# Performance work log

Measured on AMD Instinct MI355X. Metric: run time of the kernel, lower is better.

## Reference

```python
import jax, jax.numpy as jnp
import numpy as np

BOUND = 1.0
MIN_NEAR = 0.05
NUM_STEPS = 64
UP_STEPS = 64
DENSITY_SCALE = 1.0
N_RAYS = 16384
HIDDEN = 64


def setup_inputs() -> dict:
    key = jax.random.key(0)
    ks = jax.random.split(key, 8)
    # cameras hover near z=2 looking roughly toward -z so rays hit the [-1,1]^3 AABB
    rays_o = jax.random.normal(ks[0], (N_RAYS, 3), jnp.float32) * 0.1 + jnp.array([0.0, 0.0, 2.0])
    rays_d = jax.random.normal(ks[1], (N_RAYS, 3), jnp.float32) * 0.2 + jnp.array([0.0, 0.0, -1.0])
    rays_d = rays_d / jnp.linalg.norm(rays_d, axis=-1, keepdims=True)
    W1 = jax.random.normal(ks[2], (3, HIDDEN), jnp.float32) / jnp.sqrt(3.0)
    b1 = jnp.zeros((HIDDEN,), jnp.float32)
    w_sigma = jax.random.normal(ks[3], (HIDDEN, 1), jnp.float32) / jnp.sqrt(float(HIDDEN))
    b_sigma = jnp.zeros((1,), jnp.float32)
    W_rgb = jax.random.normal(ks[4], (HIDDEN, 3), jnp.float32) / jnp.sqrt(float(HIDDEN))
    b_rgb = jnp.zeros((3,), jnp.float32)
    return {"rays_o": rays_o, "rays_d": rays_d, "W1": W1, "b1": b1,
            "w_sigma": w_sigma, "b_sigma": b_sigma, "W_rgb": W_rgb, "b_rgb": b_rgb}


def near_far_cube(rays_o, rays_d, bound, min_near):
    tmin = (-bound - rays_o) / (rays_d + 1e-15)
    tmax = (bound - rays_o) / (rays_d + 1e-15)
    near = jnp.max(jnp.minimum(tmin, tmax), axis=-1, keepdims=True)
    far = jnp.min(jnp.maximum(tmin, tmax), axis=-1, keepdims=True)
    miss = far < near
    near = jnp.where(miss, 1e9, near)
    far = jnp.where(miss, 1e9, far)
    near = jnp.maximum(near, min_near)
    return near, far


def sample_pdf(bins, weights, n_samples):
    # bins: [N, M+1], weights: [N, M]; deterministic (det=True) inverse-CDF sampling
    weights = weights + 1e-5
    pdf = weights / jnp.sum(weights, -1, keepdims=True)
    cdf = jnp.cumsum(pdf, -1)
    cdf = jnp.concatenate([jnp.zeros_like(cdf[..., :1]), cdf], -1)  # [N, M+1]
    u = jnp.linspace(0.5 / n_samples, 1.0 - 0.5 / n_samples, n_samples, dtype=cdf.dtype)
    u = jnp.broadcast_to(u, cdf.shape[:-1] + (n_samples,))
    inds = jax.vmap(lambda c, uu: jnp.searchsorted(c, uu, side='right'))(cdf, u)
    below = jnp.maximum(inds - 1, 0)
    above = jnp.minimum(inds, cdf.shape[-1] - 1)
    cdf_b = jnp.take_along_axis(cdf, below, -1)
    cdf_a = jnp.take_along_axis(cdf, above, -1)
    bins_b = jnp.take_along_axis(bins, below, -1)
    bins_a = jnp.take_along_axis(bins, above, -1)
    denom = cdf_a - cdf_b
    denom = jnp.where(denom < 1e-5, jnp.ones_like(denom), denom)
    t = (u - cdf_b) / denom
    return bins_b + t * (bins_a - bins_b)


def mlp(pts, W1, b1, w_sigma, b_sigma, W_rgb, b_rgb):
    h = jax.nn.relu(pts @ W1 + b1)                      # [N, T, HIDDEN]
    sigma = jax.nn.softplus(h @ w_sigma + b_sigma)[..., 0]  # [N, T]
    rgb = jax.nn.sigmoid(h @ W_rgb + b_rgb)             # [N, T, 3]
    return sigma, rgb


def alpha_composite_weights(z_vals, sigma, sample_dist):
    deltas = z_vals[..., 1:] - z_vals[..., :-1]
    deltas = jnp.concatenate([deltas, jnp.broadcast_to(sample_dist, deltas[..., :1].shape)], -1)
    alphas = 1.0 - jnp.exp(-deltas * DENSITY_SCALE * sigma)
    trans = jnp.cumprod(jnp.concatenate([jnp.ones_like(alphas[..., :1]), 1.0 - alphas + 1e-15], -1)[..., :-1], -1)
    return alphas * trans


def reference(rays_o, rays_d, W1, b1, w_sigma, b_sigma, W_rgb, b_rgb):
    rays_d = rays_d / jnp.linalg.norm(rays_d, axis=-1, keepdims=True)
    near, far = near_far_cube(rays_o, rays_d, BOUND, MIN_NEAR)  # [N,1]
    sample_dist = (far - near) / NUM_STEPS                      # [N,1]

    # coarse stratified (deterministic) samples
    z = jnp.linspace(0.0, 1.0, NUM_STEPS, dtype=rays_o.dtype)
    z_vals = near + (far - near) * z                            # [N,T]
    xyzs = rays_o[:, None, :] + rays_d[:, None, :] * z_vals[..., None]
    xyzs = jnp.clip(xyzs, -BOUND, BOUND)
    sigma, _ = mlp(xyzs, W1, b1, w_sigma, b_sigma, W_rgb, b_rgb)
    weights = alpha_composite_weights(z_vals, sigma, sample_dist)

    # inverse-CDF importance resampling (no-grad in original)
    z_mid = 0.5 * (z_vals[..., :-1] + z_vals[..., 1:])          # [N,T-1]
    new_z = sample_pdf(z_mid, weights[:, 1:-1], UP_STEPS)       # [N,UP]
    new_z = jax.lax.stop_gradient(new_z)

    z_all = jnp.sort(jnp.concatenate([z_vals, new_z], -1), -1)  # [N,T+UP]
    xyzs_all = rays_o[:, None, :] + rays_d[:, None, :] * z_all[..., None]
    xyzs_all = jnp.clip(xyzs_all, -BOUND, BOUND)
    sigma_all, rgb_all = mlp(xyzs_all, W1, b1, w_sigma, b_sigma, W_rgb, b_rgb)
    weights_all = alpha_composite_weights(z_all, sigma_all, sample_dist)

    weights_sum = jnp.sum(weights_all, -1)                      # [N]
    image = jnp.sum(weights_all[..., None] * rgb_all, axis=-2)  # [N,3]
    image = image + (1.0 - weights_sum)[..., None]              # white background
    return image
```

## Files before the change

kernel.cpp:

```cpp
#include <hip/hip_runtime.h>
#include <math.h>

#define WAVES_PER_BLOCK 4

typedef float v2f __attribute__((ext_vector_type(2)));
typedef float v4f __attribute__((ext_vector_type(4)));
typedef __fp16 fp16v2 __attribute__((ext_vector_type(2)));
typedef _Float16 half8 __attribute__((ext_vector_type(8)));

__device__ __forceinline__ v2f v2_fma(v2f a, v2f b, v2f c) {
    return __builtin_elementwise_fma(a, b, c);
}
__device__ __forceinline__ v2f v2_max0(v2f a) {
    return __builtin_elementwise_max(a, (v2f){0.0f, 0.0f});
}
__device__ __forceinline__ v2f v2_splat(float x) { return (v2f){x, x}; }

__device__ __forceinline__ float fast_rcp(float x) { return __builtin_amdgcn_rcpf(x); }

#define DPP_ROW_SHR(n)  (0x110 | (n))
#define DPP_WF_SL1      0x130
#define DPP_WF_SR1      0x138
#define DPP_ROW_BCAST15 0x142
#define DPP_ROW_BCAST31 0x143

template <int CTRL, int RM = 0xf, int BM = 0xf, bool BC = false>
__device__ __forceinline__ float fdpp(float old_, float src) {
    return __int_as_float(__builtin_amdgcn_update_dpp(
        __float_as_int(old_), __float_as_int(src), CTRL, RM, BM, BC));
}
template <int CTRL, int RM = 0xf, int BM = 0xf, bool BC = false>
__device__ __forceinline__ int idpp(int old_, int src) {
    return __builtin_amdgcn_update_dpp(old_, src, CTRL, RM, BM, BC);
}

__device__ __forceinline__ float lane63_bcast(float x) {
    return __int_as_float(__builtin_amdgcn_readlane(__float_as_int(x), 63));
}

__device__ __forceinline__ float scan_add_dpp(float x) {
    x += fdpp<DPP_ROW_SHR(1)>(0.0f, x);
    x += fdpp<DPP_ROW_SHR(2)>(0.0f, x);
    x += fdpp<DPP_ROW_SHR(4)>(0.0f, x);
    x += fdpp<DPP_ROW_SHR(8)>(0.0f, x);
    x += fdpp<DPP_ROW_BCAST15, 0xa>(0.0f, x);
    x += fdpp<DPP_ROW_BCAST31, 0xc>(0.0f, x);
    return x;
}
__device__ __forceinline__ float scan_mul_dpp(float x) {
    x *= fdpp<DPP_ROW_SHR(1)>(1.0f, x);
    x *= fdpp<DPP_ROW_SHR(2)>(1.0f, x);
    x *= fdpp<DPP_ROW_SHR(4)>(1.0f, x);
    x *= fdpp<DPP_ROW_SHR(8)>(1.0f, x);
    x *= fdpp<DPP_ROW_BCAST15, 0xa>(1.0f, x);
    x *= fdpp<DPP_ROW_BCAST31, 0xc>(1.0f, x);
    return x;
}
__device__ __forceinline__ float wave_sum_dpp(float x) {
    return lane63_bcast(scan_add_dpp(x));
}
__device__ __forceinline__ int imax2(int a, int b) { return a > b ? a : b; }
__device__ __forceinline__ int imax_scan_dpp(int x) {
    const int NEG = (int)0x80000000;
    x = imax2(x, idpp<DPP_ROW_SHR(1)>(NEG, x));
    x = imax2(x, idpp<DPP_ROW_SHR(2)>(NEG, x));
    x = imax2(x, idpp<DPP_ROW_SHR(4)>(NEG, x));
    x = imax2(x, idpp<DPP_ROW_SHR(8)>(NEG, x));
    x = imax2(x, idpp<DPP_ROW_BCAST15, 0xa>(NEG, x));
    x = imax2(x, idpp<DPP_ROW_BCAST31, 0xc>(NEG, x));
    return x;
}

__device__ __forceinline__ float softplus_f(float x) {
    return fmaxf(x, 0.0f) + __logf(1.0f + __expf(-fabsf(x)));
}
__device__ __forceinline__ float sigmoid_f(float x) {
    return fast_rcp(1.0f + __expf(-x));
}
__device__ __forceinline__ float clamp1(float x) {
    return fminf(fmaxf(x, -1.0f), 1.0f);
}

__device__ __forceinline__ void bstage(float& a, float& b, int d, int lane) {
    float av = __shfl_xor(a, d, 64);
    float bv = __shfl_xor(b, d, 64);
    bool up = (lane & d) != 0;
    float alo = fminf(a, av), ahi = fmaxf(a, av);
    float blo = fminf(b, bv), bhi = fmaxf(b, bv);
    a = up ? ahi : alo;
    b = up ? bhi : blo;
}

__device__ __forceinline__ half8 build_afrag(const v2f* cr, const v2f* mr, v2f zz, int q) {
    union { half8 h; fp16v2 p[4]; } af;
#pragma unroll
    for (int g4 = 0; g4 < 4; ++g4) {
        v2f hp = v2_max0(v2_fma(mr[q * 4 + g4], zz, cr[q * 4 + g4]));
        af.p[g4] = __builtin_amdgcn_cvt_pkrtz(hp.x, hp.y);
    }
    return af.h;
}

__global__ __launch_bounds__(WAVES_PER_BLOCK * 64, 4)
void nerf_render_kernel(const float* __restrict__ rays_o,
                        const float* __restrict__ rays_d,
                        const float* __restrict__ W1,
                        const float* __restrict__ b1,
                        const float* __restrict__ w_sigma,
                        const float* __restrict__ b_sigma,
                        const float* __restrict__ W_rgb,
                        const float* __restrict__ b_rgb,
                        float* __restrict__ out)
{
    const int tid  = threadIdx.x;
    const int lane = tid & 63;
    const int wv   = tid >> 6;
    const int ray  = blockIdx.x * WAVES_PER_BLOCK + wv;
    const int r15  = lane & 15;
    const int kgrp = lane >> 4;

    __shared__ float s_cm [WAVES_PER_BLOCK][128];
    __shared__ int   s_scr[WAVES_PER_BLOCK][64];
    __shared__ float s_sig[WAVES_PER_BLOCK][64];
    __shared__ float s_out[WAVES_PER_BLOCK][4 * 132];

    half8 bfrag[2];
#pragma unroll
    for (int q = 0; q < 2; ++q) {
#pragma unroll
        for (int j = 0; j < 8; ++j) {
            int k = q * 32 + kgrp * 8 + j;
            float wval = 0.0f;
            if (r15 == 0)      wval = w_sigma[k];
            else if (r15 < 4)  wval = W_rgb[3 * k + (r15 - 1)];
            bfrag[q][j] = (_Float16)wval;
        }
    }

    float ox = rays_o[ray * 3 + 0], oy = rays_o[ray * 3 + 1], oz = rays_o[ray * 3 + 2];
    float dx = rays_d[ray * 3 + 0], dy = rays_d[ray * 3 + 1], dz = rays_d[ray * 3 + 2];
    {
        float inv = __builtin_amdgcn_rsqf(dx * dx + dy * dy + dz * dz);
        dx *= inv; dy *= inv; dz *= inv;
    }

    float rx = fast_rcp(dx + 1e-15f);
    float ry = fast_rcp(dy + 1e-15f);
    float rz = fast_rcp(dz + 1e-15f);
    float t0x = (-1.0f - ox) * rx, t1x = (1.0f - ox) * rx;
    float t0y = (-1.0f - oy) * ry, t1y = (1.0f - oy) * ry;
    float t0z = (-1.0f - oz) * rz, t1z = (1.0f - oz) * rz;
    float nearv = fmaxf(fmaxf(fminf(t0x, t1x), fminf(t0y, t1y)), fminf(t0z, t1z));
    float farv  = fminf(fminf(fmaxf(t0x, t1x), fmaxf(t0y, t1y)), fmaxf(t0z, t1z));
    const bool miss = (farv < nearv);
    if (miss) { nearv = 1e9f; farv = 1e9f; }
    nearv = fmaxf(nearv, 0.05f);
    const float sample_dist = (farv - nearv) * (1.0f / 64.0f);

    const float bs0 = b_sigma[0];
    const float br0 = b_rgb[0], br1 = b_rgb[1], br2 = b_rgb[2];

    {
        float w1x = W1[lane], w1y = W1[64 + lane], w1z = W1[128 + lane];
        float eox = ox, eoy = oy, eoz = oz, msc = 1.0f;
        if (miss) {
            eox = clamp1(fmaf(dx, 1e9f, ox));
            eoy = clamp1(fmaf(dy, 1e9f, oy));
            eoz = clamp1(fmaf(dz, 1e9f, oz));
            msc = 0.0f;
        }
        float cj = fmaf(eox, w1x, fmaf(eoy, w1y, fmaf(eoz, w1z, b1[lane])));
        float mj = msc * fmaf(dx, w1x, fmaf(dy, w1y, dz * w1z));
        int g = (lane >> 1) * 4 + (lane & 1);
        s_cm[wv][g]     = cj;
        s_cm[wv][g + 2] = mj;
    }

    v2f cr[8], mr[8];
#pragma unroll
    for (int q = 0; q < 2; ++q) {
#pragma unroll
        for (int g4 = 0; g4 < 4; ++g4) {
            v4f g = *(const v4f*)&s_cm[wv][4 * (q * 16 + kgrp * 4 + g4)];
            cr[q * 4 + g4] = (v2f){g.x, g.y};
            mr[q * 4 + g4] = (v2f){g.z, g.w};
        }
    }

    const float biasv = (r15 == 0) ? bs0 : (r15 == 1) ? br0 : (r15 == 2) ? br1
                       : (r15 == 3) ? br2 : 0.0f;
    const v4f accInit = (v4f){biasv, biasv, biasv, biasv};

    const float stepz = (farv - nearv) * (1.0f / 63.0f);
#pragma unroll
    for (int mt = 0; mt < 4; ++mt) {
        float zs = fminf(fmaf(stepz, (float)(mt * 16 + r15), nearv), 6.0e4f);
        v2f zz = v2_splat(zs);
        v4f acc = accInit;
        acc = __builtin_amdgcn_mfma_f32_16x16x32_f16(build_afrag(cr, mr, zz, 0), bfrag[0], acc, 0, 0, 0);
        acc = __builtin_amdgcn_mfma_f32_16x16x32_f16(build_afrag(cr, mr, zz, 1), bfrag[1], acc, 0, 0, 0);
        if (r15 == 0) {
            *(v4f*)&s_sig[wv][mt * 16 + kgrp * 4] = acc;
        }
    }
    float sigma = softplus_f(s_sig[wv][lane]);

    float z = nearv + (farv - nearv) * ((float)lane * (1.0f / 63.0f));

    float z_next = fdpp<DPP_WF_SL1>(0.0f, z);
    float delta  = (lane < 63) ? (z_next - z) : sample_dist;
    float alpha  = 1.0f - __expf(-delta * sigma);
    float v      = 1.0f - alpha + 1e-15f;
    float incl   = scan_mul_dpp(v);
    float trans  = fdpp<DPP_WF_SR1>(1.0f, incl);
    float w = alpha * trans;

    float wgt = (lane >= 1 && lane <= 62) ? (w + 1e-5f) : 0.0f;
    float cumw = scan_add_dpp(wgt);
    float total = lane63_bcast(cumw);
    float cdf_incl = cumw * fast_rcp(total);

    float cdfv  = (lane < 63) ? cdf_incl : 2.0f;
    float zmidv = (lane < 63) ? (0.5f * (z + z_next)) : 0.0f;

    int s = (int)ceilf(fmaf(64.0f, cdfv, -0.5f));
    s = s < 0 ? 0 : (s > 64 ? 64 : s);
    int snext = idpp<DPP_WF_SL1>(65, s);
    bool glast = (snext > s) && (s < 64);

    s_scr[wv][lane] = -1;
    if (glast) s_scr[wv][s] = lane;
    int below = imax_scan_dpp(s_scr[wv][lane]);
    int above = below + 1; if (above > 62) above = 62;

    float cb = __shfl(cdfv,  below, 64);
    float ca = __shfl(cdfv,  above, 64);
    float bb = __shfl(zmidv, below, 64);
    float ba = __shfl(zmidv, above, 64);
    float denom = ca - cb;
    if (denom < 1e-5f) denom = 1.0f;
    float t = (__shfl(cdfv, 0, 64) * 0.0f + (0.0078125f + (float)lane * 0.015625f) - cb) * fast_rcp(denom);
    float nz = fmaf(t, ba - bb, bb);

    float r0v = z;
    float r1v = __shfl(nz, 63 - lane, 64);
    {
        float lo = fminf(r0v, r1v), hi = fmaxf(r0v, r1v);
        r0v = lo; r1v = hi;
    }
    bstage(r0v, r1v, 32, lane);
    bstage(r0v, r1v, 16, lane);
    bstage(r0v, r1v,  8, lane);
    bstage(r0v, r1v,  4, lane);
    bstage(r0v, r1v,  2, lane);
    bstage(r0v, r1v,  1, lane);

#pragma unroll 2
    for (int mt = 0; mt < 8; ++mt) {
        const int Mbase = mt * 16;
        float zraw = (mt < 4) ? __shfl(r0v, Mbase + r15, 64)
                              : __shfl(r1v, (Mbase - 64) + r15, 64);
        float zs = fminf(zraw, 6.0e4f);
        v2f zz = v2_splat(zs);
        v4f acc = accInit;
        acc = __builtin_amdgcn_mfma_f32_16x16x32_f16(build_afrag(cr, mr, zz, 0), bfrag[0], acc, 0, 0, 0);
        acc = __builtin_amdgcn_mfma_f32_16x16x32_f16(build_afrag(cr, mr, zz, 1), bfrag[1], acc, 0, 0, 0);
        if (r15 < 4) {
            *(v4f*)&s_out[wv][r15 * 132 + Mbase + kgrp * 4] = acc;
        }
    }

    int i0 = 2 * lane, i1 = 2 * lane + 1;
    float a0r = __shfl(r0v, i0 & 63, 64), a0s = __shfl(r1v, i0 & 63, 64);
    float a1r = __shfl(r0v, i1 & 63, 64), a1s = __shfl(r1v, i1 & 63, 64);
    float za0 = (i0 < 64) ? a0r : a0s;
    float za1 = (i1 < 64) ? a1r : a1s;

    v2f sgp = *(const v2f*)&s_out[wv][0 * 132 + 2 * lane];
    v2f rp  = *(const v2f*)&s_out[wv][1 * 132 + 2 * lane];
    v2f gp  = *(const v2f*)&s_out[wv][2 * 132 + 2 * lane];
    v2f bp  = *(const v2f*)&s_out[wv][3 * 132 + 2 * lane];

    float sg0 = softplus_f(sgp.x), sg1 = softplus_f(sgp.y);
    float r0c = sigmoid_f(rp.x),   r1c = sigmoid_f(rp.y);
    float g0c = sigmoid_f(gp.x),   g1c = sigmoid_f(gp.y);
    float b0c = sigmoid_f(bp.x),   b1c = sigmoid_f(bp.y);

    float zn0 = fdpp<DPP_WF_SL1>(0.0f, za0);
    float d0 = za1 - za0;
    float d1 = (lane < 63) ? (zn0 - za1) : sample_dist;
    float aa0 = 1.0f - __expf(-d0 * sg0);
    float aa1 = 1.0f - __expf(-d1 * sg1);
    float v0 = 1.0f - aa0 + 1e-15f;
    float v1 = 1.0f - aa1 + 1e-15f;
    float local = v0 * v1;
    float incl2 = scan_mul_dpp(local);
    float eprod = fdpp<DPP_WF_SR1>(1.0f, incl2);
    float w0 = aa0 * eprod;
    float w1 = aa1 * (eprod * v0);

    float wsum = wave_sum_dpp(w0 + w1);
    float rs   = wave_sum_dpp(fmaf(w0, r0c, w1 * r1c));
    float gs   = wave_sum_dpp(fmaf(w0, g0c, w1 * g1c));
    float bs   = wave_sum_dpp(fmaf(w0, b0c, w1 * b1c));

    if (lane == 0) {
        float bg = 1.0f - wsum;
        out[ray * 3 + 0] = rs + bg;
        out[ray * 3 + 1] = gs + bg;
        out[ray * 3 + 2] = bs + bg;
    }
}

extern "C" void kernel_launch(void* const* d_in, const int* in_sizes, int n_in,
                              void* d_out, int out_size, void* d_ws, size_t ws_size,
                              hipStream_t stream) {
    const float* rays_o  = (const float*)d_in[0];
    const float* rays_d  = (const float*)d_in[1];
    const float* W1      = (const float*)d_in[2];
    const float* b1      = (const float*)d_in[3];
    const float* w_sigma = (const float*)d_in[4];
    const float* b_sigma = (const float*)d_in[5];
    const float* W_rgb   = (const float*)d_in[6];
    const float* b_rgb   = (const float*)d_in[7];
    float* out = (float*)d_out;

    const int n_rays = in_sizes[0] / 3;
    dim3 grid((n_rays + WAVES_PER_BLOCK - 1) / WAVES_PER_BLOCK);
    dim3 block(WAVES_PER_BLOCK * 64);
    hipLaunchKernelGGL(nerf_render_kernel, grid, block, 0, stream,
                       rays_o, rays_d, W1, b1, w_sigma, b_sigma, W_rgb, b_rgb, out);
}
```

Measured before the change: 98.01 us.

## Replace bitonic merge sort with rank-based merge of coarse and fine samples

The 7-stage bitonic sort of the 128 combined z values is replaced by computing each sample's final position directly. Each coarse sample's rank among the fine samples comes from evaluating the piecewise-linear CDF at its z. The fine samples then fill the remaining slots, found through OR-reduced occupancy bitmasks and a popcount select. Both sets are scattered into shared memory and read back for the MLP and compositing, which avoids many cross-lane shuffles. The risk is that ties or floating-point edge cases could place two samples in the same slot, or order them differently than a true sort.

```diff
diff --git a/kernel.cpp b/kernel.cpp
--- a/kernel.cpp
+++ b/kernel.cpp
@@ -70,6 +70,15 @@
     x = imax2(x, idpp<DPP_ROW_BCAST31, 0xc>(NEG, x));
     return x;
 }
+__device__ __forceinline__ unsigned or_reduce_u32(unsigned x) {
+    x |= (unsigned)idpp<DPP_ROW_SHR(1)>(0, (int)x);
+    x |= (unsigned)idpp<DPP_ROW_SHR(2)>(0, (int)x);
+    x |= (unsigned)idpp<DPP_ROW_SHR(4)>(0, (int)x);
+    x |= (unsigned)idpp<DPP_ROW_SHR(8)>(0, (int)x);
+    x |= (unsigned)idpp<DPP_ROW_BCAST15, 0xa>(0, (int)x);
+    x |= (unsigned)idpp<DPP_ROW_BCAST31, 0xc>(0, (int)x);
+    return (unsigned)__builtin_amdgcn_readlane((int)x, 63);
+}
 
 __device__ __forceinline__ float softplus_f(float x) {
     return fmaxf(x, 0.0f) + __logf(1.0f + __expf(-fabsf(x)));
@@ -79,16 +88,6 @@
 }
 __device__ __forceinline__ float clamp1(float x) {
     return fminf(fmaxf(x, -1.0f), 1.0f);
-}
-
-__device__ __forceinline__ void bstage(float& a, float& b, int d, int lane) {
-    float av = __shfl_xor(a, d, 64);
-    float bv = __shfl_xor(b, d, 64);
-    bool up = (lane & d) != 0;
-    float alo = fminf(a, av), ahi = fmaxf(a, av);
-    float blo = fminf(b, bv), bhi = fmaxf(b, bv);
-    a = up ? ahi : alo;
-    b = up ? bhi : blo;
 }
 
 __device__ __forceinline__ half8 build_afrag(const v2f* cr, const v2f* mr, v2f zz, int q) {
@@ -119,10 +118,11 @@
     const int r15  = lane & 15;
     const int kgrp = lane >> 4;
 
-    __shared__ float s_cm [WAVES_PER_BLOCK][128];
-    __shared__ int   s_scr[WAVES_PER_BLOCK][64];
-    __shared__ float s_sig[WAVES_PER_BLOCK][64];
-    __shared__ float s_out[WAVES_PER_BLOCK][4 * 132];
+    __shared__ float s_cm  [WAVES_PER_BLOCK][128];
+    __shared__ int   s_scr [WAVES_PER_BLOCK][64];
+    __shared__ float s_sig [WAVES_PER_BLOCK][64];
+    __shared__ float s_zall[WAVES_PER_BLOCK][128];
+    __shared__ float s_out [WAVES_PER_BLOCK][4 * 132];
 
     half8 bfrag[2];
 #pragma unroll
@@ -156,6 +156,7 @@
     if (miss) { nearv = 1e9f; farv = 1e9f; }
     nearv = fmaxf(nearv, 0.05f);
     const float sample_dist = (farv - nearv) * (1.0f / 64.0f);
+    const bool degen = !((farv - nearv) > 1e-9f);
 
     const float bs0 = b_sigma[0];
     const float br0 = b_rgb[0], br1 = b_rgb[1], br2 = b_rgb[2];
@@ -239,28 +240,56 @@
     float ba = __shfl(zmidv, above, 64);
     float denom = ca - cb;
     if (denom < 1e-5f) denom = 1.0f;
-    float t = (__shfl(cdfv, 0, 64) * 0.0f + (0.0078125f + (float)lane * 0.015625f) - cb) * fast_rcp(denom);
+    float u = 0.0078125f + (float)lane * 0.015625f;
+    float t = (u - cb) * fast_rcp(denom);
     float nz = fmaf(t, ba - bb, bb);
 
-    float r0v = z;
-    float r1v = __shfl(nz, 63 - lane, 64);
+    int pa;
     {
-        float lo = fminf(r0v, r1v), hi = fmaxf(r0v, r1v);
-        r0v = lo; r1v = hi;
-    }
-    bstage(r0v, r1v, 32, lane);
-    bstage(r0v, r1v, 16, lane);
-    bstage(r0v, r1v,  8, lane);
-    bstage(r0v, r1v,  4, lane);
-    bstage(r0v, r1v,  2, lane);
-    bstage(r0v, r1v,  1, lane);
+        float cdf_prev  = fdpp<DPP_WF_SR1>(0.0f, cdfv);
+        float zmid_prev = fdpp<DPP_WF_SR1>(0.0f, zmidv);
+        float den   = zmidv - zmid_prev;
+        float slope = (cdfv - cdf_prev) * fast_rcp(den);
+        float F     = fmaf(z - zmid_prev, slope, cdf_prev);
+        int cc = (int)ceilf(fmaf(64.0f, F, -0.5f));
+        cc = cc < 0 ? 0 : (cc > 64 ? 64 : cc);
+        int rkA = (lane == 0) ? 0 : (lane >= 63 ? 64 : cc);
+        if (degen) rkA = 0;
+        pa = lane + rkA;
+    }
+
+    int pb;
+    {
+        unsigned bit = 1u << (pa & 31);
+        int word = pa >> 5;
+        unsigned m0 = or_reduce_u32(word == 0 ? bit : 0u);
+        unsigned m1 = or_reduce_u32(word == 1 ? bit : 0u);
+        unsigned m2 = or_reduce_u32(word == 2 ? bit : 0u);
+        unsigned m3 = or_reduce_u32(word == 3 ? bit : 0u);
+        unsigned zw0 = ~m0, zw1 = ~m1, zw2 = ~m2, zw3 = ~m3;
+        int c0 = __popc(zw0), c1n = __popc(zw1), c2n = __popc(zw2);
+        int tA = c0, tB = c0 + c1n, tC = c0 + c1n + c2n;
+        int n, base; unsigned wz;
+        if (lane < tA)      { base = 0;  n = lane;      wz = zw0; }
+        else if (lane < tB) { base = 32; n = lane - tA; wz = zw1; }
+        else if (lane < tC) { base = 64; n = lane - tB; wz = zw2; }
+        else                { base = 96; n = lane - tC; wz = zw3; }
+        int off = 0, ch;
+        ch = __popc(wz & 0xFFFFu);          if (n >= ch) { n -= ch; off = 16; }
+        ch = __popc((wz >> off) & 0xFFu);   if (n >= ch) { n -= ch; off += 8; }
+        ch = __popc((wz >> off) & 0xFu);    if (n >= ch) { n -= ch; off += 4; }
+        ch = __popc((wz >> off) & 0x3u);    if (n >= ch) { n -= ch; off += 2; }
+        ch = (int)((wz >> off) & 1u);       if (n >= ch) { off += 1; }
+        pb = base + off;
+    }
+
+    s_zall[wv][pa] = z;
+    s_zall[wv][pb] = nz;
 
 #pragma unroll 2
     for (int mt = 0; mt < 8; ++mt) {
         const int Mbase = mt * 16;
-        float zraw = (mt < 4) ? __shfl(r0v, Mbase + r15, 64)
-                              : __shfl(r1v, (Mbase - 64) + r15, 64);
-        float zs = fminf(zraw, 6.0e4f);
+        float zs = fminf(s_zall[wv][Mbase + r15], 6.0e4f);
         v2f zz = v2_splat(zs);
         v4f acc = accInit;
         acc = __builtin_amdgcn_mfma_f32_16x16x32_f16(build_afrag(cr, mr, zz, 0), bfrag[0], acc, 0, 0, 0);
@@ -270,11 +299,8 @@
         }
     }
 
-    int i0 = 2 * lane, i1 = 2 * lane + 1;
-    float a0r = __shfl(r0v, i0 & 63, 64), a0s = __shfl(r1v, i0 & 63, 64);
-    float a1r = __shfl(r0v, i1 & 63, 64), a1s = __shfl(r1v, i1 & 63, 64);
-    float za0 = (i0 < 64) ? a0r : a0s;
-    float za1 = (i1 < 64) ? a1r : a1s;
+    v2f za = *(const v2f*)&s_zall[wv][2 * lane];
+    float za0 = za.x, za1 = za.y;
 
     v2f sgp = *(const v2f*)&s_out[wv][0 * 132 + 2 * lane];
     v2f rp  = *(const v2f*)&s_out[wv][1 * 132 + 2 * lane];
```

After: 98.86 us. Within noise of the previous version (+0.9%).
